# Kernel optimization log

Measured on AMD Instinct MI355X. Metric: run time of the kernel, lower is better.

Reference implementation:

```python
import jax, jax.numpy as jnp
from jax import lax
import numpy as np

B, C, H, W = 8, 192, 128, 128
HEADS, WS, SS = 6, 8, 4
HID = 768  # 4 * C
HEAD_DIM = C // HEADS
SCALE = HEAD_DIM ** -0.5
EPS = 1e-5


def _rel_pos_index(ws):
    coords = np.stack(np.meshgrid(np.arange(ws), np.arange(ws), indexing='ij'))  # (2, ws, ws)
    flat = coords.reshape(2, ws * ws)
    rel = flat[:, :, None] - flat[:, None, :]          # (2, N, N)
    rel = rel.transpose(1, 2, 0)                       # (N, N, 2)
    rel[:, :, 0] += ws - 1
    rel[:, :, 1] += ws - 1
    rel[:, :, 0] *= 2 * ws - 1
    return rel.sum(-1).astype(np.int32)                # (N, N)


def _attn_mask(hp, wp, ws, ss):
    # Swin shift mask: 0 where tokens share a region, -100 otherwise. (nW, N, N)
    img = np.zeros((hp, wp), dtype=np.float32)
    slices = (slice(0, -ws), slice(-ws, -ss), slice(-ss, None))
    cnt = 0
    for hs in slices:
        for ws_ in slices:
            img[hs, ws_] = float(cnt)
            cnt += 1
    mw = img.reshape(hp // ws, ws, wp // ws, ws).transpose(0, 2, 1, 3).reshape(-1, ws * ws)
    am = mw[:, None, :] - mw[:, :, None]
    return np.where(am != 0, -100.0, 0.0).astype(np.float32)


def _layernorm(x, g, b):
    mu = jnp.mean(x, axis=-1, keepdims=True)
    var = jnp.mean(jnp.square(x - mu), axis=-1, keepdims=True)
    return (x - mu) * lax.rsqrt(var + EPS) * g + b


def setup_inputs() -> dict:
    key = jax.random.key(0)
    ks = jax.random.split(key, 16)
    s = 0.02
    return {
        'x': jax.random.normal(ks[0], (B, C, H, W), jnp.float32),
        'pos_conv_w': jax.random.normal(ks[1], (C, 1, 3, 3), jnp.float32) * s,
        'norm1_g': jnp.ones((C,), jnp.float32),
        'norm1_b': jnp.zeros((C,), jnp.float32),
        'qkv_w': jax.random.normal(ks[2], (C, 3 * C), jnp.float32) * s,
        'qkv_b': jnp.zeros((3 * C,), jnp.float32),
        'proj_w': jax.random.normal(ks[3], (C, C), jnp.float32) * s,
        'proj_b': jnp.zeros((C,), jnp.float32),
        'rel_bias_table': jax.random.normal(ks[4], ((2 * WS - 1) ** 2, HEADS), jnp.float32) * s,
        'norm2_g': jnp.ones((C,), jnp.float32),
        'norm2_b': jnp.zeros((C,), jnp.float32),
        'mlp_w1': jax.random.normal(ks[5], (C, HID), jnp.float32) * s,
        'mlp_b1': jnp.zeros((HID,), jnp.float32),
        'mlp_w2': jax.random.normal(ks[6], (HID, C), jnp.float32) * s,
        'mlp_b2': jnp.zeros((C,), jnp.float32),
    }


def reference(x, pos_conv_w, norm1_g, norm1_b, qkv_w, qkv_b, proj_w, proj_b,
              rel_bias_table, norm2_g, norm2_b, mlp_w1, mlp_b1, mlp_w2, mlp_b2):
    b, c, h, w = x.shape
    ws, ss, nh, hd = WS, SS, HEADS, HEAD_DIM
    N = ws * ws

    # depthwise 3x3 positional conv (residual)
    x = x + lax.conv_general_dilated(
        x, pos_conv_w, (1, 1), 'SAME', feature_group_count=c,
        dimension_numbers=('NCHW', 'OIHW', 'NCHW'))

    if ss > 0:
        x = jnp.roll(x, (-ss, -ss), axis=(2, 3))

    pad_h = (ws - h % ws) % ws
    pad_w = (ws - w % ws) % ws
    if pad_h or pad_w:
        x = jnp.pad(x, ((0, 0), (0, 0), (0, pad_h), (0, pad_w)))
    hp, wp = h + pad_h, w + pad_w

    # window partition -> (num_windows, N, c)
    windows = x.reshape(b, c, hp // ws, ws, wp // ws, ws)
    windows = windows.transpose(0, 2, 4, 3, 5, 1).reshape(-1, N, c)
    nw = windows.shape[0]

    a = _layernorm(windows, norm1_g, norm1_b)
    qkv = (a @ qkv_w + qkv_b).reshape(nw, N, 3, nh, hd).transpose(2, 0, 3, 1, 4)
    q, k, v = qkv[0], qkv[1], qkv[2]                      # (nw, nh, N, hd)

    attn = jnp.einsum('whnd,whmd->whnm', q * SCALE, k)    # (nw, nh, N, N)

    rel_idx = jnp.asarray(_rel_pos_index(ws))             # (N, N) int
    bias = rel_bias_table[rel_idx.reshape(-1)].reshape(N, N, nh).transpose(2, 0, 1)
    attn = attn + bias[None]

    if ss > 0:
        mask = jnp.asarray(_attn_mask(hp, wp, ws, ss))    # (nW_per_img, N, N)
        nwpb = (hp // ws) * (wp // ws)
        attn = attn.reshape(b, nwpb, nh, N, N) + mask[None, :, None]
        attn = attn.reshape(nw, nh, N, N)

    attn = jax.nn.softmax(attn, axis=-1)
    out = jnp.einsum('whnm,whmd->whnd', attn, v).transpose(0, 2, 1, 3).reshape(nw, N, c)

    windows = windows + out @ proj_w + proj_b
    hmid = jax.nn.gelu(_layernorm(windows, norm2_g, norm2_b) @ mlp_w1 + mlp_b1, approximate=False)
    windows = windows + hmid @ mlp_w2 + mlp_b2

    # unpartition -> (b, c, hp, wp), crop, roll back
    y = windows.reshape(b, hp // ws, wp // ws, ws, ws, c)
    y = y.transpose(0, 5, 1, 3, 2, 4).reshape(b, c, hp, wp)[:, :, :h, :w]
    if ss > 0:
        y = jnp.roll(y, (ss, ss), axis=(2, 3))
    return y
```

## Files before the change

### kernel.cpp

```cpp
#include <hip/hip_runtime.h>
#include <cstdint>
#include <cstddef>

typedef short short8 __attribute__((ext_vector_type(8)));
typedef float float4_ __attribute__((ext_vector_type(4)));
typedef unsigned int uint4_ __attribute__((ext_vector_type(4)));
typedef unsigned int uint2_ __attribute__((ext_vector_type(2)));

#define DEVI static __device__ __forceinline__

DEVI unsigned short f2bf(float f) {
  union { float f; unsigned u; } v; v.f = f;
  return (unsigned short)((v.u + 0x7FFFu + ((v.u >> 16) & 1u)) >> 16);
}
DEVI unsigned pack2bf(float a, float b) {
  return (unsigned)f2bf(a) | ((unsigned)f2bf(b) << 16);
}
DEVI float bf2f(unsigned short h) {
  union { unsigned u; float f; } v; v.u = ((unsigned)h) << 16;
  return v.f;
}
DEVI float gelu_f(float x) {
  float u = x * (0.7978845608f + 0.0356774081f * x * x);
  float e = __expf(-2.0f * u);
  return x / (1.0f + e);
}

#define SCALE_Q 0.17677669529663687f

__global__ __launch_bounds__(256) void k_prep(
    const float* __restrict__ qkv_w, const float* __restrict__ qkv_b,
    const float* __restrict__ proj_w, const float* __restrict__ mlp_w1,
    const float* __restrict__ mlp_w2, const float* __restrict__ relt,
    unsigned short* __restrict__ qkvWT, unsigned short* __restrict__ projWT,
    unsigned short* __restrict__ w1T, unsigned short* __restrict__ w2T,
    float* __restrict__ qkv_b_s, float* __restrict__ bias_attn) {
  int i = blockIdx.x * 256 + threadIdx.x;
  if (i < 110592) { int n = i / 192, k = i - n * 192;
    float v = qkv_w[k * 576 + n]; if (n < 192) v *= SCALE_Q;
    qkvWT[i] = f2bf(v); return; }
  i -= 110592;
  if (i < 576) { qkv_b_s[i] = qkv_b[i] * (i < 192 ? SCALE_Q : 1.0f); return; }
  i -= 576;
  if (i < 36864) { int n = i / 192, k = i - n * 192;
    projWT[i] = f2bf(proj_w[k * 192 + n]); return; }
  i -= 36864;
  if (i < 147456) { int n = i / 192, k = i - n * 192;
    w1T[i] = f2bf(mlp_w1[k * 768 + n]); return; }
  i -= 147456;
  if (i < 147456) { int n = i / 768, k = i - n * 768;
    w2T[i] = f2bf(mlp_w2[k * 192 + n]); return; }
  i -= 147456;
  if (i < 24576) {
    int h = i >> 12, nm = i & 4095, n = nm >> 6, m = nm & 63;
    int dr = (n >> 3) - (m >> 3) + 7, dc = (n & 7) - (m & 7) + 7;
    bias_attn[i] = relt[(dr * 15 + dc) * 6 + h];
  }
}

__global__ __launch_bounds__(256) void k_conv(
    const float* __restrict__ x, const float* __restrict__ convw,
    unsigned short* __restrict__ temp) {
  __shared__ float s_in[66 * 128];
  int bx = blockIdx.x;
  int c = bx >> 1, seg = bx & 1, b = blockIdx.y;
  int h0 = seg * 64;
  int t = threadIdx.x;
  const float* xp = x + ((size_t)(b * 192 + c)) * 16384;
  #pragma unroll
  for (int i = 0; i < 9; ++i) {
    int q = t + i * 256;
    if (q < 2112) {
      int srow = q >> 5, chunk = q & 31;
      float4_ v = *(const float4_*)(xp + ((h0 + 3 + srow) & 127) * 128 + chunk * 4);
      *(float4_*)(s_in + srow * 128 + chunk * 4) = v;
    }
  }
  float cw9[9];
  #pragma unroll
  for (int i = 0; i < 9; ++i) cw9[i] = convw[c * 9 + i];
  __syncthreads();
  int r2 = t >> 7;
  int wp = t & 127;
  int w_true = (wp + 4) & 127;
  float mw0 = (w_true != 0) ? 1.f : 0.f;
  float mw2 = (w_true != 127) ? 1.f : 0.f;
  int wl0 = (w_true + 127) & 127, wl2 = (w_true + 1) & 127;
  unsigned short* tp = temp + ((size_t)(b * 192 + c)) * 16384;
  #pragma unroll 4
  for (int it = 0; it < 32; ++it) {
    int r = it * 2 + r2;
    int h_true = (h0 + 4 + r) & 127;
    float mh0 = (h_true != 0) ? 1.f : 0.f;
    float mh2 = (h_true != 127) ? 1.f : 0.f;
    const float* row0 = s_in + r * 128;
    const float* row1 = row0 + 128;
    const float* row2 = row1 + 128;
    float acc = row1[w_true];
    acc = fmaf(cw9[0], mh0 * mw0 * row0[wl0], acc);
    acc = fmaf(cw9[1], mh0 * row0[w_true], acc);
    acc = fmaf(cw9[2], mh0 * mw2 * row0[wl2], acc);
    acc = fmaf(cw9[3], mw0 * row1[wl0], acc);
    acc = fmaf(cw9[4], row1[w_true], acc);
    acc = fmaf(cw9[5], mw2 * row1[wl2], acc);
    acc = fmaf(cw9[6], mh2 * mw0 * row2[wl0], acc);
    acc = fmaf(cw9[7], mh2 * row2[w_true], acc);
    acc = fmaf(cw9[8], mh2 * mw2 * row2[wl2], acc);
    tp[(size_t)(h0 + r) * 128 + wp] = f2bf(acc);
  }
}

__global__ __launch_bounds__(256) void k_lnw(
    const unsigned short* __restrict__ temp, const float* __restrict__ g1,
    const float* __restrict__ b1, unsigned short* __restrict__ xw,
    unsigned short* __restrict__ a) {
  __shared__ unsigned short sT[192 * 128];
  __shared__ float s_g[192], s_b[192];
  int t = threadIdx.x;
  for (int i = t; i < 192; i += 256) { s_g[i] = g1[i]; s_b[i] = b1[i]; }
  int wj0 = blockIdx.x * 2, wi = blockIdx.y, b = blockIdx.z;
  const unsigned short* tb = temp + (size_t)b * (192 * 16384) + (wi * 8) * 128 + wj0 * 8;
  #pragma unroll
  for (int i = 0; i < 12; ++i) {
    int id = t + i * 256;
    int c = id >> 4, rem = id & 15, r = rem >> 1, piece = rem & 1;
    short8 v = *(const short8*)(tb + (size_t)c * 16384 + r * 128 + piece * 8);
    *(short8*)(sT + c * 128 + piece * 64 + r * 8) = v;
  }
  __syncthreads();
  int tok = t >> 1, half = t & 1, c0 = half * 96;
  size_t gtok = ((size_t)(b * 256 + wi * 16 + wj0 + (tok >> 6))) * 64 + (tok & 63);
  unsigned short* xwp = xw + gtok * 192 + c0;
  float sum = 0.f, sq = 0.f;
  #pragma unroll
  for (int j8 = 0; j8 < 12; ++j8) {
    unsigned short raw[8];
    unsigned pk[4];
    #pragma unroll
    for (int e = 0; e < 8; ++e) {
      unsigned short rv = sT[(c0 + j8 * 8 + e) * 128 + tok];
      raw[e] = rv;
      float x = bf2f(rv);
      sum += x; sq = fmaf(x, x, sq);
    }
    #pragma unroll
    for (int k = 0; k < 4; ++k) pk[k] = (unsigned)raw[2 * k] | ((unsigned)raw[2 * k + 1] << 16);
    uint4_ pv = { pk[0], pk[1], pk[2], pk[3] };
    *(uint4_*)(xwp + j8 * 8) = pv;
  }
  sum += __shfl_xor(sum, 1);
  sq  += __shfl_xor(sq, 1);
  float mu = sum * (1.f / 192.f);
  float var = sq * (1.f / 192.f) - mu * mu;
  float rs = rsqrtf(var + 1e-5f);
  unsigned short* ap = a + gtok * 192 + c0;
  #pragma unroll
  for (int j8 = 0; j8 < 12; ++j8) {
    unsigned pk[4];
    #pragma unroll
    for (int k = 0; k < 4; ++k) {
      int c = c0 + j8 * 8 + k * 2;
      float v0 = (bf2f(sT[c * 128 + tok]) - mu) * rs * s_g[c] + s_b[c];
      float v1 = (bf2f(sT[(c + 1) * 128 + tok]) - mu) * rs * s_g[c + 1] + s_b[c + 1];
      pk[k] = pack2bf(v0, v1);
    }
    uint4_ pv = { pk[0], pk[1], pk[2], pk[3] };
    *(uint4_*)(ap + j8 * 8) = pv;
  }
}

__global__ __launch_bounds__(256, 2) void k_qkv(
    const unsigned short* __restrict__ a, const unsigned short* __restrict__ wT,
    const float* __restrict__ bias, unsigned short* __restrict__ outq) {
  int t = threadIdx.x, lane = t & 63, wv = t >> 6;
  int lrow = lane & 15, lkgrp = lane >> 4, lk = lkgrp * 8;
  size_t tok0 = (size_t)blockIdx.x * 128 + (size_t)wv * 32;
  int win = (int)(tok0 >> 6), tloc0 = (int)(tok0 & 63);
  unsigned short* wbase = outq + (size_t)win * 36864;
  const unsigned short* aBase = a + tok0 * 192 + lk;
  short8 af[2][6];
  #pragma unroll
  for (int tb = 0; tb < 2; ++tb)
    #pragma unroll
    for (int ks = 0; ks < 6; ++ks)
      af[tb][ks] = *(const short8*)(aBase + (size_t)(tb * 16 + lrow) * 192 + ks * 32);
  short8 bw0[3][3], bw1[3][3];
  #pragma unroll
  for (int nb = 0; nb < 3; ++nb)
    #pragma unroll
    for (int k3 = 0; k3 < 3; ++k3)
      bw0[nb][k3] = *(const short8*)(wT + (size_t)(nb * 16 + lrow) * 192 + k3 * 32 + lk);
  #pragma unroll 1
  for (int ng = 0; ng < 12; ++ng) {
    int col0 = ng * 48;
    #pragma unroll
    for (int nb = 0; nb < 3; ++nb)
      #pragma unroll
      for (int k3 = 0; k3 < 3; ++k3)
        bw1[nb][k3] = *(const short8*)(wT + (size_t)(col0 + nb * 16 + lrow) * 192 + (3 + k3) * 32 + lk);
    float4_ acc[2][3];
    #pragma unroll
    for (int tb = 0; tb < 2; ++tb)
      #pragma unroll
      for (int nb = 0; nb < 3; ++nb) acc[tb][nb] = (float4_){0.f, 0.f, 0.f, 0.f};
    #pragma unroll
    for (int k3 = 0; k3 < 3; ++k3)
      #pragma unroll
      for (int tb = 0; tb < 2; ++tb)
        #pragma unroll
        for (int nb = 0; nb < 3; ++nb)
          acc[tb][nb] = __builtin_amdgcn_mfma_f32_16x16x32_bf16(bw0[nb][k3], af[tb][k3], acc[tb][nb], 0, 0, 0);
    if (ng < 11) {
      int nc = col0 + 48;
      #pragma unroll
      for (int nb = 0; nb < 3; ++nb)
        #pragma unroll
        for (int k3 = 0; k3 < 3; ++k3)
          bw0[nb][k3] = *(const short8*)(wT + (size_t)(nc + nb * 16 + lrow) * 192 + k3 * 32 + lk);
    }
    #pragma unroll
    for (int k3 = 0; k3 < 3; ++k3)
      #pragma unroll
      for (int tb = 0; tb < 2; ++tb)
        #pragma unroll
        for (int nb = 0; nb < 3; ++nb)
          acc[tb][nb] = __builtin_amdgcn_mfma_f32_16x16x32_bf16(bw1[nb][k3], af[tb][3 + k3], acc[tb][nb], 0, 0, 0);
    #pragma unroll
    for (int nb = 0; nb < 3; ++nb) {
      int c0 = col0 + nb * 16;
      int qkvi = c0 / 192, hd = c0 - qkvi * 192;
      int head = hd >> 5, d0 = hd & 31;
      float4_ b4 = *(const float4_*)(bias + c0 + lkgrp * 4);
      unsigned short* dst = wbase + qkvi * 12288 + head * 2048 + d0 + lkgrp * 4;
      #pragma unroll
      for (int tb = 0; tb < 2; ++tb) {
        unsigned lo = pack2bf(acc[tb][nb][0] + b4[0], acc[tb][nb][1] + b4[1]);
        unsigned hi = pack2bf(acc[tb][nb][2] + b4[2], acc[tb][nb][3] + b4[3]);
        uint2_ pv = { lo, hi };
        *(uint2_*)(dst + (size_t)(tloc0 + tb * 16 + lrow) * 32) = pv;
      }
    }
  }
}

__global__ __launch_bounds__(384, 3) void k_attn(
    const unsigned short* __restrict__ qkv, const float* __restrict__ biasAll,
    unsigned short* __restrict__ outO) {
  __shared__ __align__(16) unsigned short sVT[6][2048];
  __shared__ __align__(16) unsigned short sP[6][4096];
  int t = threadIdx.x, lane = t & 63, head = t >> 6;
  int win = blockIdx.x;
  int wi = (win >> 4) & 15, wj = win & 15;
  const unsigned short* qb = qkv + (size_t)win * 36864 + head * 2048;
  const unsigned short* kb = qb + 12288;
  const unsigned short* vb = qb + 24576;
  int lrow = lane & 15, lkgrp = lane >> 4, lk = lkgrp * 8;
  short8 kf[4];
  #pragma unroll
  for (int ni = 0; ni < 4; ++ni)
    kf[ni] = *(const short8*)(kb + (size_t)(ni * 16 + lrow) * 32 + lk);
  {
    const unsigned short* vrow = vb + (size_t)lane * 32;
    short8 vv[4];
    #pragma unroll
    for (int j = 0; j < 4; ++j) vv[j] = *(const short8*)(vrow + j * 8);
    char* vt = (char*)sVT[head];
    #pragma unroll
    for (int j = 0; j < 4; ++j)
      #pragma unroll
      for (int e = 0; e < 8; ++e) {
        int d = j * 8 + e;
        *(unsigned short*)(vt + ((d * 128 + lane * 2) ^ ((d & 7) << 4))) = (unsigned short)vv[j][e];
      }
  }
  const float* bh = biasAll + head * 4096;
  bool wi15 = (wi == 15), wj15 = (wj == 15);
  bool edge = wi15 || wj15;
  char* sp = (char*)sP[head];
  #pragma unroll
  for (int mi = 0; mi < 4; ++mi) {
    short8 qf = *(const short8*)(qb + (size_t)(mi * 16 + lrow) * 32 + lk);
    float4_ s[4];
    #pragma unroll
    for (int ni = 0; ni < 4; ++ni) {
      s[ni] = (float4_){0.f, 0.f, 0.f, 0.f};
      s[ni] = __builtin_amdgcn_mfma_f32_16x16x32_bf16(qf, kf[ni], s[ni], 0, 0, 0);
    }
    #pragma unroll
    for (int e = 0; e < 4; ++e) {
      int row = mi * 16 + lkgrp * 4 + e;
      int rcls = (wi15 ? ((row >> 3) >= 4 ? 2 : 1) : 0) * 3 +
                 (wj15 ? ((row & 7) >= 4 ? 2 : 1) : 0);
      float v[4];
      #pragma unroll
      for (int ni = 0; ni < 4; ++ni) {
        int col = ni * 16 + lrow;
        float xv = s[ni][e] + bh[row * 64 + col];
        if (edge) {
          int ccls = (wi15 ? ((col >> 3) >= 4 ? 2 : 1) : 0) * 3 +
                     (wj15 ? ((col & 7) >= 4 ? 2 : 1) : 0);
          if (ccls != rcls) xv -= 100.f;
        }
        v[ni] = xv;
      }
      float mx = fmaxf(fmaxf(v[0], v[1]), fmaxf(v[2], v[3]));
      mx = fmaxf(mx, __shfl_xor(mx, 1));
      mx = fmaxf(mx, __shfl_xor(mx, 2));
      mx = fmaxf(mx, __shfl_xor(mx, 4));
      mx = fmaxf(mx, __shfl_xor(mx, 8));
      float sm = 0.f;
      #pragma unroll
      for (int ni = 0; ni < 4; ++ni) { v[ni] = __expf(v[ni] - mx); sm += v[ni]; }
      sm += __shfl_xor(sm, 1);
      sm += __shfl_xor(sm, 2);
      sm += __shfl_xor(sm, 4);
      sm += __shfl_xor(sm, 8);
      float inv = 1.f / sm;
      #pragma unroll
      for (int ni = 0; ni < 4; ++ni) {
        int col = ni * 16 + lrow;
        *(unsigned short*)(sp + ((row * 128 + col * 2) ^ ((row & 7) << 4))) = f2bf(v[ni] * inv);
      }
    }
  }
  float4_ o[2][4];
  #pragma unroll
  for (int db = 0; db < 2; ++db)
    #pragma unroll
    for (int qb2 = 0; qb2 < 4; ++qb2) o[db][qb2] = (float4_){0.f, 0.f, 0.f, 0.f};
  char* vt = (char*)sVT[head];
  #pragma unroll
  for (int kk = 0; kk < 2; ++kk) {
    int ktok = kk * 32 + lk;
    short8 vf[2], pf[4];
    #pragma unroll
    for (int db = 0; db < 2; ++db) {
      int d = db * 16 + lrow;
      vf[db] = *(const short8*)(vt + ((d * 128 + ktok * 2) ^ ((d & 7) << 4)));
    }
    #pragma unroll
    for (int qb2 = 0; qb2 < 4; ++qb2) {
      int rq = qb2 * 16 + lrow;
      pf[qb2] = *(const short8*)(sp + ((rq * 128 + ktok * 2) ^ ((rq & 7) << 4)));
    }
    #pragma unroll
    for (int db = 0; db < 2; ++db)
      #pragma unroll
      for (int qb2 = 0; qb2 < 4; ++qb2)
        o[db][qb2] = __builtin_amdgcn_mfma_f32_16x16x32_bf16(vf[db], pf[qb2], o[db][qb2], 0, 0, 0);
  }
  unsigned short* ob = outO + (size_t)win * (64 * 192);
  #pragma unroll
  for (int qb2 = 0; qb2 < 4; ++qb2)
    #pragma unroll
    for (int db = 0; db < 2; ++db) {
      unsigned lo = pack2bf(o[db][qb2][0], o[db][qb2][1]);
      unsigned hi = pack2bf(o[db][qb2][2], o[db][qb2][3]);
      uint2_ pv = { lo, hi };
      *(uint2_*)(ob + (size_t)(qb2 * 16 + lrow) * 192 + head * 32 + db * 16 + lkgrp * 4) = pv;
    }
}

__global__ __launch_bounds__(256, 2) void k_mlp(
    const unsigned short* __restrict__ O, const unsigned short* __restrict__ xw,
    const unsigned short* __restrict__ projWT, const float* __restrict__ proj_b,
    const float* __restrict__ n2g, const float* __restrict__ n2b,
    const unsigned short* __restrict__ w1T, const float* __restrict__ mlpb1,
    const unsigned short* __restrict__ w2T, const float* __restrict__ mlpb2,
    float* __restrict__ y) {
  __shared__ __align__(16) unsigned short sH[64 * 192];
  __shared__ __align__(16) unsigned short sB2[64 * 192];
  __shared__ float sRed[64 * 8];
  int t = threadIdx.x, lane = t & 63, wn = t >> 6;
  int lrow = lane & 15, lkgrp = lane >> 4, lk = lkgrp * 8;
  int win = blockIdx.x;
  const unsigned short* obase = O + (size_t)win * (64 * 192);
  float4_ tacc[4][3];
  #pragma unroll
  for (int mi = 0; mi < 4; ++mi)
    #pragma unroll
    for (int ni = 0; ni < 3; ++ni) tacc[mi][ni] = (float4_){0.f, 0.f, 0.f, 0.f};
  {
    short8 bP0[3][3], bP1[3][3], af0[4], af1[4];
    #pragma unroll
    for (int ni = 0; ni < 3; ++ni)
      #pragma unroll
      for (int k3 = 0; k3 < 3; ++k3)
        bP0[ni][k3] = *(const short8*)(projWT + (size_t)(wn * 48 + ni * 16 + lrow) * 192 + k3 * 32 + lk);
    #pragma unroll
    for (int mi = 0; mi < 4; ++mi)
      af0[mi] = *(const short8*)(obase + (size_t)(mi * 16 + lrow) * 192 + lk);
    #pragma unroll
    for (int ni = 0; ni < 3; ++ni)
      #pragma unroll
      for (int k3 = 0; k3 < 3; ++k3)
        bP1[ni][k3] = *(const short8*)(projWT + (size_t)(wn * 48 + ni * 16 + lrow) * 192 + (3 + k3) * 32 + lk);
    #pragma unroll
    for (int mi = 0; mi < 4; ++mi)
      af1[mi] = *(const short8*)(obase + (size_t)(mi * 16 + lrow) * 192 + 32 + lk);
    #pragma unroll
    for (int ks = 0; ks < 6; ++ks) {
      #pragma unroll
      for (int mi = 0; mi < 4; ++mi) {
        short8 a_ = (ks & 1) ? af1[mi] : af0[mi];
        #pragma unroll
        for (int ni = 0; ni < 3; ++ni) {
          short8 b_ = (ks < 3) ? bP0[ni][ks] : bP1[ni][ks - 3];
          tacc[mi][ni] = __builtin_amdgcn_mfma_f32_16x16x32_bf16(a_, b_, tacc[mi][ni], 0, 0, 0);
        }
      }
      if (ks < 4) {
        #pragma unroll
        for (int mi = 0; mi < 4; ++mi) {
          short8 nv = *(const short8*)(obase + (size_t)(mi * 16 + lrow) * 192 + (ks + 2) * 32 + lk);
          if (ks & 1) af1[mi] = nv; else af0[mi] = nv;
        }
      }
    }
  }
  {
    unsigned short rxv[3][4][4];
    #pragma unroll
    for (int ni = 0; ni < 3; ++ni) {
      int col = wn * 48 + ni * 16 + lrow;
      #pragma unroll
      for (int mi = 0; mi < 4; ++mi)
        #pragma unroll
        for (int e = 0; e < 4; ++e)
          rxv[ni][mi][e] = xw[((size_t)win * 64 + mi * 16 + lkgrp * 4 + e) * 192 + col];
    }
    #pragma unroll
    for (int ni = 0; ni < 3; ++ni) {
      float pbv = proj_b[wn * 48 + ni * 16 + lrow];
      #pragma unroll
      for (int mi = 0; mi < 4; ++mi)
        #pragma unroll
        for (int e = 0; e < 4; ++e)
          tacc[mi][ni][e] += pbv + bf2f(rxv[ni][mi][e]);
    }
  }
  #pragma unroll
  for (int mi = 0; mi < 4; ++mi)
    #pragma unroll
    for (int e = 0; e < 4; ++e) {
      float s1 = tacc[mi][0][e] + tacc[mi][1][e] + tacc[mi][2][e];
      float s2 = tacc[mi][0][e] * tacc[mi][0][e] + tacc[mi][1][e] * tacc[mi][1][e] +
                 tacc[mi][2][e] * tacc[mi][2][e];
      s1 += __shfl_xor(s1, 1); s1 += __shfl_xor(s1, 2); s1 += __shfl_xor(s1, 4); s1 += __shfl_xor(s1, 8);
      s2 += __shfl_xor(s2, 1); s2 += __shfl_xor(s2, 2); s2 += __shfl_xor(s2, 4); s2 += __shfl_xor(s2, 8);
      if (lrow == 0) {
        int row = mi * 16 + lkgrp * 4 + e;
        sRed[row * 8 + wn * 2 + 0] = s1;
        sRed[row * 8 + wn * 2 + 1] = s2;
      }
    }
  __syncthreads();
  #pragma unroll
  for (int mi = 0; mi < 4; ++mi)
    #pragma unroll
    for (int e = 0; e < 4; ++e) {
      int row = mi * 16 + lkgrp * 4 + e;
      float s1 = sRed[row * 8] + sRed[row * 8 + 2] + sRed[row * 8 + 4] + sRed[row * 8 + 6];
      float s2 = sRed[row * 8 + 1] + sRed[row * 8 + 3] + sRed[row * 8 + 5] + sRed[row * 8 + 7];
      float mu = s1 * (1.f / 192.f);
      float var = s2 * (1.f / 192.f) - mu * mu;
      float rs = rsqrtf(var + 1e-5f);
      #pragma unroll
      for (int ni = 0; ni < 3; ++ni) {
        int col = wn * 48 + ni * 16 + lrow;
        float hv = (tacc[mi][ni][e] - mu) * rs * n2g[col] + n2b[col];
        *(unsigned short*)((char*)sH + ((row * 384 + col * 2) ^ ((row & 7) << 4))) = f2bf(hv);
      }
    }
  __syncthreads();
  short8 bwA[6], bwB[6];
  #pragma unroll
  for (int ks = 0; ks < 6; ++ks)
    bwA[ks] = *(const short8*)(w1T + (size_t)(wn * 48 + lrow) * 192 + ks * 32 + lk);
  #pragma unroll 1
  for (int ch = 0; ch < 4; ++ch) {
    #pragma unroll 1
    for (int ni = 0; ni < 3; ++ni) {
      int nni = (ni < 2) ? ni + 1 : 0;
      int nch = (ni < 2) ? ch : ch + 1;
      if (nch < 4) {
        int gn = nch * 192 + wn * 48 + nni * 16 + lrow;
        #pragma unroll
        for (int ks = 0; ks < 6; ++ks)
          bwB[ks] = *(const short8*)(w1T + (size_t)gn * 192 + ks * 32 + lk);
      }
      float4_ h1[4];
      #pragma unroll
      for (int mi = 0; mi < 4; ++mi) h1[mi] = (float4_){0.f, 0.f, 0.f, 0.f};
      #pragma unroll
      for (int ks = 0; ks < 6; ++ks) {
        int kb = ks * 32 + lk;
        #pragma unroll
        for (int mi = 0; mi < 4; ++mi) {
          int row = mi * 16 + lrow;
          short8 afv = *(const short8*)((const char*)sH + ((row * 384 + kb * 2) ^ ((row & 7) << 4)));
          h1[mi] = __builtin_amdgcn_mfma_f32_16x16x32_bf16(afv, bwA[ks], h1[mi], 0, 0, 0);
        }
      }
      float b1v = mlpb1[ch * 192 + wn * 48 + ni * 16 + lrow];
      int col = wn * 48 + ni * 16 + lrow;
      #pragma unroll
      for (int mi = 0; mi < 4; ++mi)
        #pragma unroll
        for (int e = 0; e < 4; ++e) {
          float v = gelu_f(h1[mi][e] + b1v);
          int row = mi * 16 + lkgrp * 4 + e;
          *(unsigned short*)((char*)sB2 + ((row * 384 + col * 2) ^ ((row & 7) << 4))) = f2bf(v);
        }
      #pragma unroll
      for (int ks = 0; ks < 6; ++ks) bwA[ks] = bwB[ks];
    }
    short8 cw0[3][3], cw1[3][3];
    #pragma unroll
    for (int ni = 0; ni < 3; ++ni)
      #pragma unroll
      for (int k3 = 0; k3 < 3; ++k3)
        cw0[ni][k3] = *(const short8*)(w2T + (size_t)(wn * 48 + ni * 16 + lrow) * 768 + ch * 192 + k3 * 32 + lk);
    __syncthreads();
    #pragma unroll
    for (int ni = 0; ni < 3; ++ni)
      #pragma unroll
      for (int k3 = 0; k3 < 3; ++k3)
        cw1[ni][k3] = *(const short8*)(w2T + (size_t)(wn * 48 + ni * 16 + lrow) * 768 + ch * 192 + (3 + k3) * 32 + lk);
    #pragma unroll
    for (int ks = 0; ks < 6; ++ks) {
      int kb = ks * 32 + lk;
      short8 af[4];
      #pragma unroll
      for (int mi = 0; mi < 4; ++mi) {
        int row = mi * 16 + lrow;
        af[mi] = *(const short8*)((const char*)sB2 + ((row * 384 + kb * 2) ^ ((row & 7) << 4)));
      }
      #pragma unroll
      for (int mi = 0; mi < 4; ++mi)
        #pragma unroll
        for (int ni = 0; ni < 3; ++ni) {
          short8 b_ = (ks < 3) ? cw0[ni][ks] : cw1[ni][ks - 3];
          tacc[mi][ni] = __builtin_amdgcn_mfma_f32_16x16x32_bf16(af[mi], b_, tacc[mi][ni], 0, 0, 0);
        }
    }
    __syncthreads();
  }
  int b = win >> 8, wi = (win >> 4) & 15, wj = win & 15;
  int r_off = lkgrp >> 1;
  int wbase = (wj * 8 + 4 + (lkgrp & 1) * 4) & 127;
  #pragma unroll
  for (int ni = 0; ni < 3; ++ni) {
    int col = wn * 48 + ni * 16 + lrow;
    float b2v = mlpb2[col];
    #pragma unroll
    for (int mi = 0; mi < 4; ++mi) {
      int r = mi * 2 + r_off;
      int h = (wi * 8 + r + 4) & 127;
      float4_ vv;
      #pragma unroll
      for (int e = 0; e < 4; ++e) vv[e] = tacc[mi][ni][e] + b2v;
      *(float4_*)(y + ((size_t)(b * 192 + col) * 128 + h) * 128 + wbase) = vv;
    }
  }
}

extern "C" void kernel_launch(void* const* d_in, const int* in_sizes, int n_in,
                              void* d_out, int out_size, void* d_ws, size_t ws_size,
                              hipStream_t stream) {
  (void)in_sizes; (void)n_in; (void)out_size;
  const float* x    = (const float*)d_in[0];
  const float* pcw  = (const float*)d_in[1];
  const float* n1g  = (const float*)d_in[2];
  const float* n1b  = (const float*)d_in[3];
  const float* qkvw = (const float*)d_in[4];
  const float* qkvb = (const float*)d_in[5];
  const float* pw   = (const float*)d_in[6];
  const float* pb   = (const float*)d_in[7];
  const float* relt = (const float*)d_in[8];
  const float* n2g  = (const float*)d_in[9];
  const float* n2b  = (const float*)d_in[10];
  const float* w1   = (const float*)d_in[11];
  const float* mb1  = (const float*)d_in[12];
  const float* w2   = (const float*)d_in[13];
  const float* mb2  = (const float*)d_in[14];
  float* y = (float*)d_out;
  char* ws = (char*)d_ws;
  size_t off = 0;
  auto carve = [&](size_t bytes) { void* p = ws + off; off += (bytes + 255) & ~(size_t)255; return p; };
  unsigned short* qkvWT  = (unsigned short*)carve(576 * 192 * 2);
  unsigned short* projWT = (unsigned short*)carve(192 * 192 * 2);
  unsigned short* w1T    = (unsigned short*)carve(768 * 192 * 2);
  unsigned short* w2T    = (unsigned short*)carve(192 * 768 * 2);
  float* qkv_b_s   = (float*)carve(576 * 4);
  float* bias_attn = (float*)carve(6 * 64 * 64 * 4);
  unsigned short* aBuf   = (unsigned short*)carve((size_t)131072 * 192 * 2);
  unsigned short* xwBuf  = (unsigned short*)carve((size_t)131072 * 192 * 2);
  unsigned short* qkvBuf = (unsigned short*)carve((size_t)131072 * 576 * 2);
  unsigned short* temp   = qkvBuf;
  if (off > ws_size) return;

  k_prep<<<dim3(1827), dim3(256), 0, stream>>>(qkvw, qkvb, pw, w1, w2, relt,
                                               qkvWT, projWT, w1T, w2T, qkv_b_s, bias_attn);
  k_conv<<<dim3(384, 8), dim3(256), 0, stream>>>(x, pcw, temp);
  k_lnw<<<dim3(8, 16, 8), dim3(256), 0, stream>>>(temp, n1g, n1b, xwBuf, aBuf);
  k_qkv<<<dim3(1024), dim3(256), 0, stream>>>(aBuf, qkvWT, qkv_b_s, qkvBuf);
  k_attn<<<dim3(2048), dim3(384), 0, stream>>>(qkvBuf, bias_attn, aBuf);
  k_mlp<<<dim3(2048), dim3(256), 0, stream>>>(aBuf, xwBuf, projWT, pb, n2g, n2b,
                                              w1T, mb1, w2T, mb2, y);
}
```

Measured before the change: 572.5 us.

## Remap MLP kernel to output-tile token gather with 8 waves per block

The fused proj+LN2+MLP kernel now gives each block a 4x16 spatial output tile instead of one window. Token indices are gathered through a shared-memory lookup that accounts for the roll, so each row of the final fp32 store is contiguous over 16 pixels and no longer wraps across the window shift. Block size doubles to 512 threads and the 64 rows are split across two wave-rows. The register-prefetched weight double-buffering is removed in favour of per-k loads, which lowers register pressure but exposes more global-load latency.

```diff
diff --git a/kernel.cpp b/kernel.cpp
--- a/kernel.cpp
+++ b/kernel.cpp
@@ -361,7 +361,7 @@
     }
 }
 
-__global__ __launch_bounds__(256, 2) void k_mlp(
+__global__ __launch_bounds__(512, 2) void k_mlp(
     const unsigned short* __restrict__ O, const unsigned short* __restrict__ xw,
     const unsigned short* __restrict__ projWT, const float* __restrict__ proj_b,
     const float* __restrict__ n2g, const float* __restrict__ n2b,
@@ -371,76 +371,65 @@
   __shared__ __align__(16) unsigned short sH[64 * 192];
   __shared__ __align__(16) unsigned short sB2[64 * 192];
   __shared__ float sRed[64 * 8];
-  int t = threadIdx.x, lane = t & 63, wn = t >> 6;
+  __shared__ unsigned sTok[64];
+  int t = threadIdx.x, lane = t & 63, wv = t >> 6;
+  int wm = wv >> 2, wn = wv & 3;
   int lrow = lane & 15, lkgrp = lane >> 4, lk = lkgrp * 8;
-  int win = blockIdx.x;
-  const unsigned short* obase = O + (size_t)win * (64 * 192);
-  float4_ tacc[4][3];
-  #pragma unroll
-  for (int mi = 0; mi < 4; ++mi)
+  int blk = blockIdx.x;
+  int b = blk >> 8, rem = blk & 255, ta = rem >> 3, tb_ = rem & 7;
+  if (t < 64) {
+    int rr = t >> 4, ss = t & 15;
+    int h = ta * 4 + rr, w = tb_ * 16 + ss;
+    int hp = (h + 124) & 127, wp = (w + 124) & 127;
+    unsigned gtok = ((unsigned)(b * 256 + (hp >> 3) * 16 + (wp >> 3))) * 64 +
+                    (hp & 7) * 8 + (wp & 7);
+    sTok[t] = gtok * 192u;
+  }
+  __syncthreads();
+  float4_ tacc[2][3];
+  #pragma unroll
+  for (int mi = 0; mi < 2; ++mi)
     #pragma unroll
     for (int ni = 0; ni < 3; ++ni) tacc[mi][ni] = (float4_){0.f, 0.f, 0.f, 0.f};
+  unsigned aoff[2];
+  #pragma unroll
+  for (int mi = 0; mi < 2; ++mi) aoff[mi] = sTok[wm * 32 + mi * 16 + lrow];
+  #pragma unroll
+  for (int ks = 0; ks < 6; ++ks) {
+    int kb = ks * 32 + lk;
+    short8 af[2], bf[3];
+    #pragma unroll
+    for (int mi = 0; mi < 2; ++mi)
+      af[mi] = *(const short8*)(O + aoff[mi] + kb);
+    #pragma unroll
+    for (int ni = 0; ni < 3; ++ni)
+      bf[ni] = *(const short8*)(projWT + (size_t)(wn * 48 + ni * 16 + lrow) * 192 + kb);
+    #pragma unroll
+    for (int mi = 0; mi < 2; ++mi)
+      #pragma unroll
+      for (int ni = 0; ni < 3; ++ni)
+        tacc[mi][ni] = __builtin_amdgcn_mfma_f32_16x16x32_bf16(af[mi], bf[ni], tacc[mi][ni], 0, 0, 0);
+  }
   {
-    short8 bP0[3][3], bP1[3][3], af0[4], af1[4];
-    #pragma unroll
-    for (int ni = 0; ni < 3; ++ni)
-      #pragma unroll
-      for (int k3 = 0; k3 < 3; ++k3)
-        bP0[ni][k3] = *(const short8*)(projWT + (size_t)(wn * 48 + ni * 16 + lrow) * 192 + k3 * 32 + lk);
-    #pragma unroll
-    for (int mi = 0; mi < 4; ++mi)
-      af0[mi] = *(const short8*)(obase + (size_t)(mi * 16 + lrow) * 192 + lk);
-    #pragma unroll
-    for (int ni = 0; ni < 3; ++ni)
-      #pragma unroll
-      for (int k3 = 0; k3 < 3; ++k3)
-        bP1[ni][k3] = *(const short8*)(projWT + (size_t)(wn * 48 + ni * 16 + lrow) * 192 + (3 + k3) * 32 + lk);
-    #pragma unroll
-    for (int mi = 0; mi < 4; ++mi)
-      af1[mi] = *(const short8*)(obase + (size_t)(mi * 16 + lrow) * 192 + 32 + lk);
-    #pragma unroll
-    for (int ks = 0; ks < 6; ++ks) {
-      #pragma unroll
-      for (int mi = 0; mi < 4; ++mi) {
-        short8 a_ = (ks & 1) ? af1[mi] : af0[mi];
-        #pragma unroll
-        for (int ni = 0; ni < 3; ++ni) {
-          short8 b_ = (ks < 3) ? bP0[ni][ks] : bP1[ni][ks - 3];
-          tacc[mi][ni] = __builtin_amdgcn_mfma_f32_16x16x32_bf16(a_, b_, tacc[mi][ni], 0, 0, 0);
-        }
-      }
-      if (ks < 4) {
-        #pragma unroll
-        for (int mi = 0; mi < 4; ++mi) {
-          short8 nv = *(const short8*)(obase + (size_t)(mi * 16 + lrow) * 192 + (ks + 2) * 32 + lk);
-          if (ks & 1) af1[mi] = nv; else af0[mi] = nv;
-        }
-      }
-    }
-  }
-  {
-    unsigned short rxv[3][4][4];
+    unsigned roff[2][4];
+    #pragma unroll
+    for (int mi = 0; mi < 2; ++mi)
+      #pragma unroll
+      for (int e = 0; e < 4; ++e)
+        roff[mi][e] = sTok[wm * 32 + mi * 16 + lkgrp * 4 + e];
     #pragma unroll
     for (int ni = 0; ni < 3; ++ni) {
       int col = wn * 48 + ni * 16 + lrow;
-      #pragma unroll
-      for (int mi = 0; mi < 4; ++mi)
+      float pbv = proj_b[col];
+      #pragma unroll
+      for (int mi = 0; mi < 2; ++mi)
         #pragma unroll
         for (int e = 0; e < 4; ++e)
-          rxv[ni][mi][e] = xw[((size_t)win * 64 + mi * 16 + lkgrp * 4 + e) * 192 + col];
-    }
-    #pragma unroll
-    for (int ni = 0; ni < 3; ++ni) {
-      float pbv = proj_b[wn * 48 + ni * 16 + lrow];
-      #pragma unroll
-      for (int mi = 0; mi < 4; ++mi)
-        #pragma unroll
-        for (int e = 0; e < 4; ++e)
-          tacc[mi][ni][e] += pbv + bf2f(rxv[ni][mi][e]);
-    }
-  }
-  #pragma unroll
-  for (int mi = 0; mi < 4; ++mi)
+          tacc[mi][ni][e] += pbv + bf2f(xw[roff[mi][e] + col]);
+    }
+  }
+  #pragma unroll
+  for (int mi = 0; mi < 2; ++mi)
     #pragma unroll
     for (int e = 0; e < 4; ++e) {
       float s1 = tacc[mi][0][e] + tacc[mi][1][e] + tacc[mi][2][e];
@@ -449,17 +438,17 @@
       s1 += __shfl_xor(s1, 1); s1 += __shfl_xor(s1, 2); s1 += __shfl_xor(s1, 4); s1 += __shfl_xor(s1, 8);
       s2 += __shfl_xor(s2, 1); s2 += __shfl_xor(s2, 2); s2 += __shfl_xor(s2, 4); s2 += __shfl_xor(s2, 8);
       if (lrow == 0) {
-        int row = mi * 16 + lkgrp * 4 + e;
+        int row = wm * 32 + mi * 16 + lkgrp * 4 + e;
         sRed[row * 8 + wn * 2 + 0] = s1;
         sRed[row * 8 + wn * 2 + 1] = s2;
       }
     }
   __syncthreads();
   #pragma unroll
-  for (int mi = 0; mi < 4; ++mi)
+  for (int mi = 0; mi < 2; ++mi)
     #pragma unroll
     for (int e = 0; e < 4; ++e) {
-      int row = mi * 16 + lkgrp * 4 + e;
+      int row = wm * 32 + mi * 16 + lkgrp * 4 + e;
       float s1 = sRed[row * 8] + sRed[row * 8 + 2] + sRed[row * 8 + 4] + sRed[row * 8 + 6];
       float s2 = sRed[row * 8 + 1] + sRed[row * 8 + 3] + sRed[row * 8 + 5] + sRed[row * 8 + 7];
       float mu = s1 * (1.f / 192.f);
@@ -473,94 +462,69 @@
       }
     }
   __syncthreads();
-  short8 bwA[6], bwB[6];
-  #pragma unroll
-  for (int ks = 0; ks < 6; ++ks)
-    bwA[ks] = *(const short8*)(w1T + (size_t)(wn * 48 + lrow) * 192 + ks * 32 + lk);
   #pragma unroll 1
   for (int ch = 0; ch < 4; ++ch) {
     #pragma unroll 1
     for (int ni = 0; ni < 3; ++ni) {
-      int nni = (ni < 2) ? ni + 1 : 0;
-      int nch = (ni < 2) ? ch : ch + 1;
-      if (nch < 4) {
-        int gn = nch * 192 + wn * 48 + nni * 16 + lrow;
-        #pragma unroll
-        for (int ks = 0; ks < 6; ++ks)
-          bwB[ks] = *(const short8*)(w1T + (size_t)gn * 192 + ks * 32 + lk);
-      }
-      float4_ h1[4];
-      #pragma unroll
-      for (int mi = 0; mi < 4; ++mi) h1[mi] = (float4_){0.f, 0.f, 0.f, 0.f};
+      int gn = ch * 192 + wn * 48 + ni * 16 + lrow;
+      float4_ h1[2];
+      #pragma unroll
+      for (int mi = 0; mi < 2; ++mi) h1[mi] = (float4_){0.f, 0.f, 0.f, 0.f};
       #pragma unroll
       for (int ks = 0; ks < 6; ++ks) {
         int kb = ks * 32 + lk;
-        #pragma unroll
-        for (int mi = 0; mi < 4; ++mi) {
-          int row = mi * 16 + lrow;
+        short8 bwv = *(const short8*)(w1T + (size_t)gn * 192 + kb);
+        #pragma unroll
+        for (int mi = 0; mi < 2; ++mi) {
+          int row = wm * 32 + mi * 16 + lrow;
           short8 afv = *(const short8*)((const char*)sH + ((row * 384 + kb * 2) ^ ((row & 7) << 4)));
-          h1[mi] = __builtin_amdgcn_mfma_f32_16x16x32_bf16(afv, bwA[ks], h1[mi], 0, 0, 0);
+          h1[mi] = __builtin_amdgcn_mfma_f32_16x16x32_bf16(afv, bwv, h1[mi], 0, 0, 0);
         }
       }
-      float b1v = mlpb1[ch * 192 + wn * 48 + ni * 16 + lrow];
+      float b1v = mlpb1[gn];
       int col = wn * 48 + ni * 16 + lrow;
       #pragma unroll
-      for (int mi = 0; mi < 4; ++mi)
+      for (int mi = 0; mi < 2; ++mi)
         #pragma unroll
         for (int e = 0; e < 4; ++e) {
           float v = gelu_f(h1[mi][e] + b1v);
-          int row = mi * 16 + lkgrp * 4 + e;
+          int row = wm * 32 + mi * 16 + lkgrp * 4 + e;
           *(unsigned short*)((char*)sB2 + ((row * 384 + col * 2) ^ ((row & 7) << 4))) = f2bf(v);
         }
-      #pragma unroll
-      for (int ks = 0; ks < 6; ++ks) bwA[ks] = bwB[ks];
-    }
-    short8 cw0[3][3], cw1[3][3];
-    #pragma unroll
-    for (int ni = 0; ni < 3; ++ni)
-      #pragma unroll
-      for (int k3 = 0; k3 < 3; ++k3)
-        cw0[ni][k3] = *(const short8*)(w2T + (size_t)(wn * 48 + ni * 16 + lrow) * 768 + ch * 192 + k3 * 32 + lk);
+    }
     __syncthreads();
-    #pragma unroll
-    for (int ni = 0; ni < 3; ++ni)
-      #pragma unroll
-      for (int k3 = 0; k3 < 3; ++k3)
-        cw1[ni][k3] = *(const short8*)(w2T + (size_t)(wn * 48 + ni * 16 + lrow) * 768 + ch * 192 + (3 + k3) * 32 + lk);
     #pragma unroll
     for (int ks = 0; ks < 6; ++ks) {
       int kb = ks * 32 + lk;
-      short8 af[4];
-      #pragma unroll
-      for (int mi = 0; mi < 4; ++mi) {
-        int row = mi * 16 + lrow;
+      short8 af[2], cw[3];
+      #pragma unroll
+      for (int mi = 0; mi < 2; ++mi) {
+        int row = wm * 32 + mi * 16 + lrow;
         af[mi] = *(const short8*)((const char*)sB2 + ((row * 384 + kb * 2) ^ ((row & 7) << 4)));
       }
       #pragma unroll
-      for (int mi = 0; mi < 4; ++mi)
-        #pragma unroll
-        for (int ni = 0; ni < 3; ++ni) {
-          short8 b_ = (ks < 3) ? cw0[ni][ks] : cw1[ni][ks - 3];
-          tacc[mi][ni] = __builtin_amdgcn_mfma_f32_16x16x32_bf16(af[mi], b_, tacc[mi][ni], 0, 0, 0);
-        }
+      for (int ni = 0; ni < 3; ++ni)
+        cw[ni] = *(const short8*)(w2T + (size_t)(wn * 48 + ni * 16 + lrow) * 768 + ch * 192 + kb);
+      #pragma unroll
+      for (int mi = 0; mi < 2; ++mi)
+        #pragma unroll
+        for (int ni = 0; ni < 3; ++ni)
+          tacc[mi][ni] = __builtin_amdgcn_mfma_f32_16x16x32_bf16(af[mi], cw[ni], tacc[mi][ni], 0, 0, 0);
     }
     __syncthreads();
   }
-  int b = win >> 8, wi = (win >> 4) & 15, wj = win & 15;
-  int r_off = lkgrp >> 1;
-  int wbase = (wj * 8 + 4 + (lkgrp & 1) * 4) & 127;
+  int wcol = tb_ * 16 + lkgrp * 4;
   #pragma unroll
   for (int ni = 0; ni < 3; ++ni) {
     int col = wn * 48 + ni * 16 + lrow;
     float b2v = mlpb2[col];
     #pragma unroll
-    for (int mi = 0; mi < 4; ++mi) {
-      int r = mi * 2 + r_off;
-      int h = (wi * 8 + r + 4) & 127;
+    for (int mi = 0; mi < 2; ++mi) {
+      int h = ta * 4 + wm * 2 + mi;
       float4_ vv;
       #pragma unroll
       for (int e = 0; e < 4; ++e) vv[e] = tacc[mi][ni][e] + b2v;
-      *(float4_*)(y + ((size_t)(b * 192 + col) * 128 + h) * 128 + wbase) = vv;
+      *(float4_*)(y + ((size_t)(b * 192 + col) * 128 + h) * 128 + wcol) = vv;
     }
   }
 }
@@ -606,6 +570,6 @@
   k_lnw<<<dim3(8, 16, 8), dim3(256), 0, stream>>>(temp, n1g, n1b, xwBuf, aBuf);
   k_qkv<<<dim3(1024), dim3(256), 0, stream>>>(aBuf, qkvWT, qkv_b_s, qkvBuf);
   k_attn<<<dim3(2048), dim3(384), 0, stream>>>(qkvBuf, bias_attn, aBuf);
-  k_mlp<<<dim3(2048), dim3(256), 0, stream>>>(aBuf, xwBuf, projWT, pb, n2g, n2b,
+  k_mlp<<<dim3(2048), dim3(512), 0, stream>>>(aBuf, xwBuf, projWT, pb, n2g, n2b,
                                               w1T, mb1, w2T, mb2, y);
 }
```

New measurement: 648.8 us. 13.3% more time.

## Fuse QKV projection into attention kernel and remap MLP tiles to output rows

Applied to the files above, without the earlier changes.

The QKV GEMM now runs inside the attention kernel. Each head wave computes its own Q, K and V for the window directly into shared memory, reusing the P buffer region for Q/K. This removes the 150MB-class bf16 qkv round trip through global memory and one kernel launch. The MLP kernel now processes 4x16 spatial tiles in output image order, gathering tokens through a shared index table, so the final y stores are more contiguous. The cost is that the input A rows are re-read per head in the attention kernel and the MLP loads become gathered.

```diff
diff --git a/kernel.cpp b/kernel.cpp
--- a/kernel.cpp
+++ b/kernel.cpp
@@ -169,123 +169,101 @@
   }
 }
 
-__global__ __launch_bounds__(256, 2) void k_qkv(
+__global__ __launch_bounds__(384, 3) void k_qkvattn(
     const unsigned short* __restrict__ a, const unsigned short* __restrict__ wT,
-    const float* __restrict__ bias, unsigned short* __restrict__ outq) {
-  int t = threadIdx.x, lane = t & 63, wv = t >> 6;
-  int lrow = lane & 15, lkgrp = lane >> 4, lk = lkgrp * 8;
-  size_t tok0 = (size_t)blockIdx.x * 128 + (size_t)wv * 32;
-  int win = (int)(tok0 >> 6), tloc0 = (int)(tok0 & 63);
-  unsigned short* wbase = outq + (size_t)win * 36864;
-  const unsigned short* aBase = a + tok0 * 192 + lk;
-  short8 af[2][6];
-  #pragma unroll
-  for (int tb = 0; tb < 2; ++tb)
-    #pragma unroll
-    for (int ks = 0; ks < 6; ++ks)
-      af[tb][ks] = *(const short8*)(aBase + (size_t)(tb * 16 + lrow) * 192 + ks * 32);
-  short8 bw0[3][3], bw1[3][3];
-  #pragma unroll
-  for (int nb = 0; nb < 3; ++nb)
-    #pragma unroll
-    for (int k3 = 0; k3 < 3; ++k3)
-      bw0[nb][k3] = *(const short8*)(wT + (size_t)(nb * 16 + lrow) * 192 + k3 * 32 + lk);
-  #pragma unroll 1
-  for (int ng = 0; ng < 12; ++ng) {
-    int col0 = ng * 48;
-    #pragma unroll
-    for (int nb = 0; nb < 3; ++nb)
-      #pragma unroll
-      for (int k3 = 0; k3 < 3; ++k3)
-        bw1[nb][k3] = *(const short8*)(wT + (size_t)(col0 + nb * 16 + lrow) * 192 + (3 + k3) * 32 + lk);
-    float4_ acc[2][3];
-    #pragma unroll
-    for (int tb = 0; tb < 2; ++tb)
-      #pragma unroll
-      for (int nb = 0; nb < 3; ++nb) acc[tb][nb] = (float4_){0.f, 0.f, 0.f, 0.f};
-    #pragma unroll
-    for (int k3 = 0; k3 < 3; ++k3)
-      #pragma unroll
-      for (int tb = 0; tb < 2; ++tb)
-        #pragma unroll
-        for (int nb = 0; nb < 3; ++nb)
-          acc[tb][nb] = __builtin_amdgcn_mfma_f32_16x16x32_bf16(bw0[nb][k3], af[tb][k3], acc[tb][nb], 0, 0, 0);
-    if (ng < 11) {
-      int nc = col0 + 48;
-      #pragma unroll
-      for (int nb = 0; nb < 3; ++nb)
-        #pragma unroll
-        for (int k3 = 0; k3 < 3; ++k3)
-          bw0[nb][k3] = *(const short8*)(wT + (size_t)(nc + nb * 16 + lrow) * 192 + k3 * 32 + lk);
-    }
-    #pragma unroll
-    for (int k3 = 0; k3 < 3; ++k3)
-      #pragma unroll
-      for (int tb = 0; tb < 2; ++tb)
-        #pragma unroll
-        for (int nb = 0; nb < 3; ++nb)
-          acc[tb][nb] = __builtin_amdgcn_mfma_f32_16x16x32_bf16(bw1[nb][k3], af[tb][3 + k3], acc[tb][nb], 0, 0, 0);
-    #pragma unroll
-    for (int nb = 0; nb < 3; ++nb) {
-      int c0 = col0 + nb * 16;
-      int qkvi = c0 / 192, hd = c0 - qkvi * 192;
-      int head = hd >> 5, d0 = hd & 31;
-      float4_ b4 = *(const float4_*)(bias + c0 + lkgrp * 4);
-      unsigned short* dst = wbase + qkvi * 12288 + head * 2048 + d0 + lkgrp * 4;
-      #pragma unroll
-      for (int tb = 0; tb < 2; ++tb) {
-        unsigned lo = pack2bf(acc[tb][nb][0] + b4[0], acc[tb][nb][1] + b4[1]);
-        unsigned hi = pack2bf(acc[tb][nb][2] + b4[2], acc[tb][nb][3] + b4[3]);
-        uint2_ pv = { lo, hi };
-        *(uint2_*)(dst + (size_t)(tloc0 + tb * 16 + lrow) * 32) = pv;
-      }
-    }
-  }
-}
-
-__global__ __launch_bounds__(384, 3) void k_attn(
-    const unsigned short* __restrict__ qkv, const float* __restrict__ biasAll,
+    const float* __restrict__ qbias, const float* __restrict__ biasAll,
     unsigned short* __restrict__ outO) {
+  __shared__ __align__(16) unsigned short sQK[6][4096];
   __shared__ __align__(16) unsigned short sVT[6][2048];
-  __shared__ __align__(16) unsigned short sP[6][4096];
-  int t = threadIdx.x, lane = t & 63, head = t >> 6;
+  int t = threadIdx.x, lane = t & 63, head = t / 64;
   int win = blockIdx.x;
   int wi = (win >> 4) & 15, wj = win & 15;
-  const unsigned short* qb = qkv + (size_t)win * 36864 + head * 2048;
-  const unsigned short* kb = qb + 12288;
-  const unsigned short* vb = qb + 24576;
   int lrow = lane & 15, lkgrp = lane >> 4, lk = lkgrp * 8;
+  const unsigned short* aWin = a + (size_t)win * (64 * 192);
+  char* qk = (char*)sQK[head];
+  char* vt = (char*)sVT[head];
+
+  auto gemmQKV = [&](int sel) {
+    const unsigned short* wb = wT + (size_t)(sel * 192 + head * 32) * 192;
+    const float* bb = qbias + sel * 192 + head * 32;
+    short8 bw[2][6];
+    #pragma unroll
+    for (int nb = 0; nb < 2; ++nb)
+      #pragma unroll
+      for (int ks = 0; ks < 6; ++ks)
+        bw[nb][ks] = *(const short8*)(wb + (size_t)(nb * 16 + lrow) * 192 + ks * 32 + lk);
+    float4_ acc[2][4];
+    #pragma unroll
+    for (int nb = 0; nb < 2; ++nb)
+      #pragma unroll
+      for (int mi = 0; mi < 4; ++mi) acc[nb][mi] = (float4_){0.f, 0.f, 0.f, 0.f};
+    short8 af0[4], af1[4];
+    #pragma unroll
+    for (int mi = 0; mi < 4; ++mi)
+      af0[mi] = *(const short8*)(aWin + (size_t)(mi * 16 + lrow) * 192 + lk);
+    #pragma unroll
+    for (int mi = 0; mi < 4; ++mi)
+      af1[mi] = *(const short8*)(aWin + (size_t)(mi * 16 + lrow) * 192 + 32 + lk);
+    #pragma unroll
+    for (int ks = 0; ks < 6; ++ks) {
+      #pragma unroll
+      for (int mi = 0; mi < 4; ++mi) {
+        short8 a_ = (ks & 1) ? af1[mi] : af0[mi];
+        #pragma unroll
+        for (int nb = 0; nb < 2; ++nb)
+          acc[nb][mi] = __builtin_amdgcn_mfma_f32_16x16x32_bf16(a_, bw[nb][ks], acc[nb][mi], 0, 0, 0);
+      }
+      if (ks < 4) {
+        #pragma unroll
+        for (int mi = 0; mi < 4; ++mi) {
+          short8 nv = *(const short8*)(aWin + (size_t)(mi * 16 + lrow) * 192 + (ks + 2) * 32 + lk);
+          if (ks & 1) af1[mi] = nv; else af0[mi] = nv;
+        }
+      }
+    }
+    #pragma unroll
+    for (int nb = 0; nb < 2; ++nb) {
+      float bv = bb[nb * 16 + lrow];
+      int d = nb * 16 + lrow;
+      #pragma unroll
+      for (int mi = 0; mi < 4; ++mi)
+        #pragma unroll
+        for (int e = 0; e < 4; ++e) {
+          unsigned short pv = f2bf(acc[nb][mi][e] + bv);
+          int tok = mi * 16 + lkgrp * 4 + e;
+          if (sel == 2)
+            *(unsigned short*)(vt + ((d * 128 + tok * 2) ^ ((d & 7) << 4))) = pv;
+          else
+            *(unsigned short*)(qk + sel * 4096 + ((tok * 64 + d * 2) ^ ((tok & 7) << 4))) = pv;
+        }
+    }
+  };
+  gemmQKV(0);
+  gemmQKV(1);
+  gemmQKV(2);
+
   short8 kf[4];
   #pragma unroll
-  for (int ni = 0; ni < 4; ++ni)
-    kf[ni] = *(const short8*)(kb + (size_t)(ni * 16 + lrow) * 32 + lk);
-  {
-    const unsigned short* vrow = vb + (size_t)lane * 32;
-    short8 vv[4];
-    #pragma unroll
-    for (int j = 0; j < 4; ++j) vv[j] = *(const short8*)(vrow + j * 8);
-    char* vt = (char*)sVT[head];
-    #pragma unroll
-    for (int j = 0; j < 4; ++j)
-      #pragma unroll
-      for (int e = 0; e < 8; ++e) {
-        int d = j * 8 + e;
-        *(unsigned short*)(vt + ((d * 128 + lane * 2) ^ ((d & 7) << 4))) = (unsigned short)vv[j][e];
-      }
+  for (int ni = 0; ni < 4; ++ni) {
+    int tokk = ni * 16 + lrow;
+    kf[ni] = *(const short8*)(qk + 4096 + ((tokk * 64 + lk * 2) ^ ((tokk & 7) << 4)));
+  }
+  float4_ s[4][4];
+  #pragma unroll
+  for (int mi = 0; mi < 4; ++mi) {
+    int tokq = mi * 16 + lrow;
+    short8 qf = *(const short8*)(qk + ((tokq * 64 + lk * 2) ^ ((tokq & 7) << 4)));
+    #pragma unroll
+    for (int ni = 0; ni < 4; ++ni) {
+      s[mi][ni] = (float4_){0.f, 0.f, 0.f, 0.f};
+      s[mi][ni] = __builtin_amdgcn_mfma_f32_16x16x32_bf16(qf, kf[ni], s[mi][ni], 0, 0, 0);
+    }
   }
   const float* bh = biasAll + head * 4096;
   bool wi15 = (wi == 15), wj15 = (wj == 15);
   bool edge = wi15 || wj15;
-  char* sp = (char*)sP[head];
   #pragma unroll
   for (int mi = 0; mi < 4; ++mi) {
-    short8 qf = *(const short8*)(qb + (size_t)(mi * 16 + lrow) * 32 + lk);
-    float4_ s[4];
-    #pragma unroll
-    for (int ni = 0; ni < 4; ++ni) {
-      s[ni] = (float4_){0.f, 0.f, 0.f, 0.f};
-      s[ni] = __builtin_amdgcn_mfma_f32_16x16x32_bf16(qf, kf[ni], s[ni], 0, 0, 0);
-    }
     #pragma unroll
     for (int e = 0; e < 4; ++e) {
       int row = mi * 16 + lkgrp * 4 + e;
@@ -295,7 +273,7 @@
       #pragma unroll
       for (int ni = 0; ni < 4; ++ni) {
         int col = ni * 16 + lrow;
-        float xv = s[ni][e] + bh[row * 64 + col];
+        float xv = s[mi][ni][e] + bh[row * 64 + col];
         if (edge) {
           int ccls = (wi15 ? ((col >> 3) >= 4 ? 2 : 1) : 0) * 3 +
                      (wj15 ? ((col & 7) >= 4 ? 2 : 1) : 0);
@@ -319,7 +297,7 @@
       #pragma unroll
       for (int ni = 0; ni < 4; ++ni) {
         int col = ni * 16 + lrow;
-        *(unsigned short*)(sp + ((row * 128 + col * 2) ^ ((row & 7) << 4))) = f2bf(v[ni] * inv);
+        *(unsigned short*)(qk + ((row * 128 + col * 2) ^ ((row & 7) << 4))) = f2bf(v[ni] * inv);
       }
     }
   }
@@ -328,7 +306,6 @@
   for (int db = 0; db < 2; ++db)
     #pragma unroll
     for (int qb2 = 0; qb2 < 4; ++qb2) o[db][qb2] = (float4_){0.f, 0.f, 0.f, 0.f};
-  char* vt = (char*)sVT[head];
   #pragma unroll
   for (int kk = 0; kk < 2; ++kk) {
     int ktok = kk * 32 + lk;
@@ -341,7 +318,7 @@
     #pragma unroll
     for (int qb2 = 0; qb2 < 4; ++qb2) {
       int rq = qb2 * 16 + lrow;
-      pf[qb2] = *(const short8*)(sp + ((rq * 128 + ktok * 2) ^ ((rq & 7) << 4)));
+      pf[qb2] = *(const short8*)(qk + ((rq * 128 + ktok * 2) ^ ((rq & 7) << 4)));
     }
     #pragma unroll
     for (int db = 0; db < 2; ++db)
@@ -371,10 +348,23 @@
   __shared__ __align__(16) unsigned short sH[64 * 192];
   __shared__ __align__(16) unsigned short sB2[64 * 192];
   __shared__ float sRed[64 * 8];
+  __shared__ unsigned sTok[64];
   int t = threadIdx.x, lane = t & 63, wn = t >> 6;
   int lrow = lane & 15, lkgrp = lane >> 4, lk = lkgrp * 8;
-  int win = blockIdx.x;
-  const unsigned short* obase = O + (size_t)win * (64 * 192);
+  int blk = blockIdx.x;
+  int b = blk >> 8, rem = blk & 255, ta = rem >> 3, tb_ = rem & 7;
+  if (t < 64) {
+    int rr = t >> 4, ss = t & 15;
+    int h = ta * 4 + rr, w = tb_ * 16 + ss;
+    int hp = (h + 124) & 127, wp = (w + 124) & 127;
+    unsigned gtok = ((unsigned)(b * 256 + (hp >> 3) * 16 + (wp >> 3))) * 64 +
+                    (hp & 7) * 8 + (wp & 7);
+    sTok[t] = gtok * 192u;
+  }
+  __syncthreads();
+  unsigned aoff[4];
+  #pragma unroll
+  for (int mi = 0; mi < 4; ++mi) aoff[mi] = sTok[mi * 16 + lrow];
   float4_ tacc[4][3];
   #pragma unroll
   for (int mi = 0; mi < 4; ++mi)
@@ -389,7 +379,7 @@
         bP0[ni][k3] = *(const short8*)(projWT + (size_t)(wn * 48 + ni * 16 + lrow) * 192 + k3 * 32 + lk);
     #pragma unroll
     for (int mi = 0; mi < 4; ++mi)
-      af0[mi] = *(const short8*)(obase + (size_t)(mi * 16 + lrow) * 192 + lk);
+      af0[mi] = *(const short8*)(O + aoff[mi] + lk);
     #pragma unroll
     for (int ni = 0; ni < 3; ++ni)
       #pragma unroll
@@ -397,7 +387,7 @@
         bP1[ni][k3] = *(const short8*)(projWT + (size_t)(wn * 48 + ni * 16 + lrow) * 192 + (3 + k3) * 32 + lk);
     #pragma unroll
     for (int mi = 0; mi < 4; ++mi)
-      af1[mi] = *(const short8*)(obase + (size_t)(mi * 16 + lrow) * 192 + 32 + lk);
+      af1[mi] = *(const short8*)(O + aoff[mi] + 32 + lk);
     #pragma unroll
     for (int ks = 0; ks < 6; ++ks) {
       #pragma unroll
@@ -412,13 +402,19 @@
       if (ks < 4) {
         #pragma unroll
         for (int mi = 0; mi < 4; ++mi) {
-          short8 nv = *(const short8*)(obase + (size_t)(mi * 16 + lrow) * 192 + (ks + 2) * 32 + lk);
+          short8 nv = *(const short8*)(O + aoff[mi] + (ks + 2) * 32 + lk);
           if (ks & 1) af1[mi] = nv; else af0[mi] = nv;
         }
       }
     }
   }
   {
+    unsigned roff[4][4];
+    #pragma unroll
+    for (int mi = 0; mi < 4; ++mi)
+      #pragma unroll
+      for (int e = 0; e < 4; ++e)
+        roff[mi][e] = sTok[mi * 16 + lkgrp * 4 + e];
     unsigned short rxv[3][4][4];
     #pragma unroll
     for (int ni = 0; ni < 3; ++ni) {
@@ -427,7 +423,7 @@
       for (int mi = 0; mi < 4; ++mi)
         #pragma unroll
         for (int e = 0; e < 4; ++e)
-          rxv[ni][mi][e] = xw[((size_t)win * 64 + mi * 16 + lkgrp * 4 + e) * 192 + col];
+          rxv[ni][mi][e] = xw[roff[mi][e] + col];
     }
     #pragma unroll
     for (int ni = 0; ni < 3; ++ni) {
@@ -546,21 +542,18 @@
     }
     __syncthreads();
   }
-  int b = win >> 8, wi = (win >> 4) & 15, wj = win & 15;
-  int r_off = lkgrp >> 1;
-  int wbase = (wj * 8 + 4 + (lkgrp & 1) * 4) & 127;
+  int wcol = tb_ * 16 + lkgrp * 4;
   #pragma unroll
   for (int ni = 0; ni < 3; ++ni) {
     int col = wn * 48 + ni * 16 + lrow;
     float b2v = mlpb2[col];
     #pragma unroll
     for (int mi = 0; mi < 4; ++mi) {
-      int r = mi * 2 + r_off;
-      int h = (wi * 8 + r + 4) & 127;
+      int h = ta * 4 + mi;
       float4_ vv;
       #pragma unroll
       for (int e = 0; e < 4; ++e) vv[e] = tacc[mi][ni][e] + b2v;
-      *(float4_*)(y + ((size_t)(b * 192 + col) * 128 + h) * 128 + wbase) = vv;
+      *(float4_*)(y + ((size_t)(b * 192 + col) * 128 + h) * 128 + wcol) = vv;
     }
   }
 }
@@ -596,16 +589,14 @@
   float* bias_attn = (float*)carve(6 * 64 * 64 * 4);
   unsigned short* aBuf   = (unsigned short*)carve((size_t)131072 * 192 * 2);
   unsigned short* xwBuf  = (unsigned short*)carve((size_t)131072 * 192 * 2);
-  unsigned short* qkvBuf = (unsigned short*)carve((size_t)131072 * 576 * 2);
-  unsigned short* temp   = qkvBuf;
+  unsigned short* temp   = (unsigned short*)carve((size_t)131072 * 192 * 2);
   if (off > ws_size) return;
 
   k_prep<<<dim3(1827), dim3(256), 0, stream>>>(qkvw, qkvb, pw, w1, w2, relt,
                                                qkvWT, projWT, w1T, w2T, qkv_b_s, bias_attn);
   k_conv<<<dim3(384, 8), dim3(256), 0, stream>>>(x, pcw, temp);
   k_lnw<<<dim3(8, 16, 8), dim3(256), 0, stream>>>(temp, n1g, n1b, xwBuf, aBuf);
-  k_qkv<<<dim3(1024), dim3(256), 0, stream>>>(aBuf, qkvWT, qkv_b_s, qkvBuf);
-  k_attn<<<dim3(2048), dim3(384), 0, stream>>>(qkvBuf, bias_attn, aBuf);
-  k_mlp<<<dim3(2048), dim3(256), 0, stream>>>(aBuf, xwBuf, projWT, pb, n2g, n2b,
+  k_qkvattn<<<dim3(2048), dim3(384), 0, stream>>>(aBuf, qkvWT, qkv_b_s, bias_attn, temp);
+  k_mlp<<<dim3(2048), dim3(256), 0, stream>>>(temp, xwBuf, projWT, pb, n2g, n2b,
                                               w1T, mb1, w2T, mb2, y);
 }
```

Result: faster. 525.9 us (-8.1%).
